# Optimization experiments

Measured on AMD Instinct MI355X. Metric: run time of the kernel, lower is better.

Reference implementation:

```python
import jax, jax.numpy as jnp
import numpy as np

B, T, D_IN, H = 32, 2048, 512, 512


def setup_inputs() -> dict:
    key = jax.random.key(0)
    ks = jax.random.split(key, 5)
    limit_z = float(np.sqrt(6.0 / (D_IN + H)))  # xavier_uniform
    return {
        "x": jax.random.normal(ks[0], (B, T, D_IN), dtype=jnp.float32),
        "motion_mag": jax.random.uniform(ks[1], (B, T), dtype=jnp.float32),
        "Wz": jax.random.uniform(ks[2], (H, D_IN), minval=-limit_z, maxval=limit_z, dtype=jnp.float32),
        "bz": jnp.full((H,), -2.0, dtype=jnp.float32),
        "Wh": jax.random.uniform(ks[3], (H, D_IN), minval=-limit_z, maxval=limit_z, dtype=jnp.float32),
        "bh": jnp.zeros((H,), dtype=jnp.float32),
        "motion_weight": jnp.asarray(1.0, dtype=jnp.float32),
        "motion_bias": jnp.asarray(0.0, dtype=jnp.float32),
        "alpha": jnp.asarray(0.5, dtype=jnp.float32),
    }


def reference(x, motion_mag, Wz, bz, Wh, bh, motion_weight, motion_bias, alpha):
    # motion-conditioned gate temperature: (B, T, 1)
    a = jax.nn.softplus(alpha)
    tau = 1.0 + a * jax.nn.sigmoid(motion_weight * motion_mag + motion_bias)
    tau = tau[..., None]
    # parallel gate / candidate projections
    z = jax.nn.sigmoid((jnp.einsum('btd,hd->bth', x, Wz) + bz) / tau)  # (B,T,H)
    h_tilde = jnp.einsum('btd,hd->bth', x, Wh) + bh                     # (B,T,H)
    # sequential elementwise recurrence: h = (1-z)*h + z*h_tilde
    h0 = jnp.zeros((x.shape[0], Wz.shape[0]), dtype=x.dtype)

    def step(h, zt_ht):
        z_t, ht_t = zt_ht
        h = (1.0 - z_t) * h + z_t * ht_t
        return h, h

    _, outs = jax.lax.scan(step, h0, (jnp.swapaxes(z, 0, 1), jnp.swapaxes(h_tilde, 0, 1)))
    return jnp.swapaxes(outs, 0, 1)  # (B, T, H)
```

## Files before the change

kernel.cpp:

```cpp
#include <hip/hip_runtime.h>
#include <math.h>

#define BATCH 32
#define TLEN 2048
#define DIN 512
#define HDIM 512
#define BTROWS (BATCH * TLEN)

typedef __attribute__((ext_vector_type(8))) short short8;
typedef __attribute__((ext_vector_type(4))) float f32x4;

__device__ __forceinline__ float sigmoidf_(float v) {
    return 1.0f / (1.0f + __expf(-v));
}

__device__ __forceinline__ unsigned short bf16_rne(float f) {
    unsigned int u = __float_as_uint(f);
    u += 0x7FFFu + ((u >> 16) & 1u);
    return (unsigned short)(u >> 16);
}

__device__ __forceinline__ void conv_body(const float* src, int t, size_t tile,
                                          short* Hs, short* Ls,
                                          short* __restrict__ dhi, short* __restrict__ dlo) {
    const int row = t >> 1, half = t & 1;
    float v[16];
#pragma unroll
    for (int i = 0; i < 4; ++i)
        *(float4*)&v[i * 4] = *(const float4*)(src + i * 4);
    const int s = row >> 4, r = row & 15;
#pragma unroll
    for (int jj = 0; jj < 2; ++jj) {
        short8 hv, lv;
#pragma unroll
        for (int e = 0; e < 8; ++e) {
            const float f = v[jj * 8 + e];
            const unsigned short h = bf16_rne(f);
            const float hf = __uint_as_float(((unsigned int)h) << 16);
            hv[e] = (short)h;
            lv[e] = (short)bf16_rne(f - hf);
        }
        const int idx = s * 512 + (half * 2 + jj) * 128 + r * 8;
        *(short8*)&Hs[idx] = hv;
        *(short8*)&Ls[idx] = lv;
    }
    __syncthreads();
    const size_t ob = tile * 4096 + (size_t)t * 16;
    *(short8*)(dhi + ob)     = *(short8*)&Hs[t * 16];
    *(short8*)(dhi + ob + 8) = *(short8*)&Hs[t * 16 + 8];
    *(short8*)(dlo + ob)     = *(short8*)&Ls[t * 16];
    *(short8*)(dlo + ob + 8) = *(short8*)&Ls[t * 16 + 8];
}

__global__ __launch_bounds__(256) void convert_x_kernel(const float* __restrict__ x,
                                                        short* __restrict__ xhi,
                                                        short* __restrict__ xlo) {
    __shared__ short Hs[4096], Ls[4096];
    const int tile = blockIdx.x;
    const int rt = tile >> 4, kt = tile & 15;
    const int t = threadIdx.x;
    const int row = t >> 1, half = t & 1;
    const float* src = x + (size_t)(rt * 128 + row) * DIN + kt * 32 + half * 16;
    conv_body(src, t, (size_t)tile, Hs, Ls, xhi, xlo);
}

__global__ __launch_bounds__(256) void convert_w_kernel(const float* __restrict__ Wz,
                                                        const float* __restrict__ Wh,
                                                        short* __restrict__ whi,
                                                        short* __restrict__ wlo) {
    __shared__ short Hs[4096], Ls[4096];
    const int tile = blockIdx.x;
    const int ct = tile >> 4, kt = tile & 15;
    const int t = threadIdx.x;
    const int row = t >> 1, half = t & 1;
    const int wrow = ct * 128 + row;
    const float* base = (wrow < HDIM) ? (Wz + (size_t)wrow * DIN)
                                      : (Wh + (size_t)(wrow - HDIM) * DIN);
    const float* src = base + kt * 32 + half * 16;
    conv_body(src, t, (size_t)tile, Hs, Ls, whi, wlo);
}

#define GLOAD16(g, l) __builtin_amdgcn_global_load_lds(                         \
    (const __attribute__((address_space(1))) unsigned int*)(g),                 \
    (__attribute__((address_space(3))) unsigned int*)(l), 16, 0, 0)

__global__ __launch_bounds__(256) void gemm_mfma_kernel(
    const short* __restrict__ xhi, const short* __restrict__ xlo,
    const short* __restrict__ whi, const short* __restrict__ wlo,
    const float* __restrict__ bz, const float* __restrict__ bh,
    const float* __restrict__ mag,
    const float* __restrict__ mw_p, const float* __restrict__ mb_p,
    const float* __restrict__ al_p,
    float* __restrict__ zbuf, float* __restrict__ out)
{
    __shared__ short Ah[4096], Al[4096], Bh[4096], Bl[4096];

    const int orig = blockIdx.x;
    const int xcd = orig & 7, idx = orig >> 3;
    const int wg = xcd * 512 + idx;
    const int bj = wg & 7;
    const int bi = wg >> 3;

    const int tid = threadIdx.x;
    const int w = tid >> 6, l = tid & 63;
    const int wr = w >> 1, wc = w & 1;

    f32x4 acc[4][4];
#pragma unroll
    for (int i = 0; i < 4; ++i)
#pragma unroll
        for (int j = 0; j < 4; ++j) acc[i][j] = (f32x4)0.f;

    const size_t ab = (size_t)bi * (16 * 4096);
    const size_t bb = (size_t)bj * (16 * 4096);
    const int c0 = tid, c1 = tid + 256;
    const int lb0 = (w * 64) * 8;
    const int lb1 = (256 + w * 64) * 8;

    for (int kt = 0; kt < 16; ++kt) {
        const size_t ta = ab + (size_t)kt * 4096;
        const size_t tb = bb + (size_t)kt * 4096;
        GLOAD16(xhi + ta + c0 * 8, &Ah[lb0]);
        GLOAD16(xhi + ta + c1 * 8, &Ah[lb1]);
        GLOAD16(xlo + ta + c0 * 8, &Al[lb0]);
        GLOAD16(xlo + ta + c1 * 8, &Al[lb1]);
        GLOAD16(whi + tb + c0 * 8, &Bh[lb0]);
        GLOAD16(whi + tb + c1 * 8, &Bh[lb1]);
        GLOAD16(wlo + tb + c0 * 8, &Bl[lb0]);
        GLOAD16(wlo + tb + c1 * 8, &Bl[lb1]);
        __syncthreads();

        short8 av[4], aw[4], bv[4], bw[4];
#pragma unroll
        for (int i = 0; i < 4; ++i) {
            av[i] = *(const short8*)&Ah[(wr * 4 + i) * 512 + l * 8];
            aw[i] = *(const short8*)&Al[(wr * 4 + i) * 512 + l * 8];
            bv[i] = *(const short8*)&Bh[(wc * 4 + i) * 512 + l * 8];
            bw[i] = *(const short8*)&Bl[(wc * 4 + i) * 512 + l * 8];
        }
#pragma unroll
        for (int i = 0; i < 4; ++i)
#pragma unroll
            for (int j = 0; j < 4; ++j) {
                acc[i][j] = __builtin_amdgcn_mfma_f32_16x16x32_bf16(av[i], bv[j], acc[i][j], 0, 0, 0);
                acc[i][j] = __builtin_amdgcn_mfma_f32_16x16x32_bf16(aw[i], bv[j], acc[i][j], 0, 0, 0);
                acc[i][j] = __builtin_amdgcn_mfma_f32_16x16x32_bf16(av[i], bw[j], acc[i][j], 0, 0, 0);
            }
        __syncthreads();
    }

    const float mwv = *mw_p, mbv = *mb_p, alv = *al_p;
    const float asp = fmaxf(alv, 0.f) + log1pf(__expf(-fabsf(alv)));
    const int colbase = bj * 128 + wc * 64 + (l & 15);
    const int rowbase = bi * 128 + wr * 64 + ((l >> 4) << 2);

    if (bj < 4) {
        float itau[4][4];
#pragma unroll
        for (int i = 0; i < 4; ++i)
#pragma unroll
            for (int q = 0; q < 4; ++q) {
                const int row = rowbase + i * 16 + q;
                const float tau = 1.0f + asp * sigmoidf_(mwv * mag[row] + mbv);
                itau[i][q] = 1.0f / tau;
            }
#pragma unroll
        for (int j = 0; j < 4; ++j) {
            const int col = colbase + j * 16;
            const float bzv = bz[col];
#pragma unroll
            for (int i = 0; i < 4; ++i)
#pragma unroll
                for (int q = 0; q < 4; ++q) {
                    const int row = rowbase + i * 16 + q;
                    zbuf[(size_t)row * HDIM + col] = sigmoidf_((acc[i][j][q] + bzv) * itau[i][q]);
                }
        }
    } else {
#pragma unroll
        for (int j = 0; j < 4; ++j) {
            const int col = colbase + j * 16 - HDIM;
            const float bhv = bh[col];
#pragma unroll
            for (int i = 0; i < 4; ++i)
#pragma unroll
                for (int q = 0; q < 4; ++q) {
                    const int row = rowbase + i * 16 + q;
                    out[(size_t)row * HDIM + col] = acc[i][j][q] + bhv;
                }
        }
    }
}

#define BM 128
#define BN 128
#define BK 16
#define TM 8
#define TN 8

__global__ __launch_bounds__(256) void gemm_dual_kernel(
    const float* __restrict__ x, const float* __restrict__ Wz, const float* __restrict__ Wh,
    const float* __restrict__ bz, const float* __restrict__ bh, const float* __restrict__ mag,
    const float* __restrict__ mw_p, const float* __restrict__ mb_p, const float* __restrict__ al_p,
    float* __restrict__ zbuf, float* __restrict__ htbuf)
{
    __shared__ float As[BK][BM + 4];
    __shared__ float Zs[BK][BN + 4];
    __shared__ float Hs[BK][BN + 4];

    const int bj = blockIdx.x, bi = blockIdx.y;
    const int tid = threadIdx.x;
    const int tx = tid & 15, ty = tid >> 4;
    const int row0 = bi * BM, col0 = bj * BN;

    float accZ[TM][TN], accH[TM][TN];
#pragma unroll
    for (int i = 0; i < TM; ++i)
#pragma unroll
        for (int j = 0; j < TN; ++j) { accZ[i][j] = 0.f; accH[i][j] = 0.f; }

    const int srow = tid >> 1;
    const int skc = (tid & 1) * 8;
    const float* xg = x + (size_t)(row0 + srow) * DIN + skc;
    const float* wzg = Wz + (size_t)(col0 + srow) * DIN + skc;
    const float* whg = Wh + (size_t)(col0 + srow) * DIN + skc;

    for (int k0 = 0; k0 < DIN; k0 += BK) {
        const float4 a0 = *(const float4*)(xg + k0);
        const float4 a1 = *(const float4*)(xg + k0 + 4);
        const float4 z0 = *(const float4*)(wzg + k0);
        const float4 z1 = *(const float4*)(wzg + k0 + 4);
        const float4 h0 = *(const float4*)(whg + k0);
        const float4 h1 = *(const float4*)(whg + k0 + 4);
        __syncthreads();
        As[skc + 0][srow] = a0.x; As[skc + 1][srow] = a0.y; As[skc + 2][srow] = a0.z; As[skc + 3][srow] = a0.w;
        As[skc + 4][srow] = a1.x; As[skc + 5][srow] = a1.y; As[skc + 6][srow] = a1.z; As[skc + 7][srow] = a1.w;
        Zs[skc + 0][srow] = z0.x; Zs[skc + 1][srow] = z0.y; Zs[skc + 2][srow] = z0.z; Zs[skc + 3][srow] = z0.w;
        Zs[skc + 4][srow] = z1.x; Zs[skc + 5][srow] = z1.y; Zs[skc + 6][srow] = z1.z; Zs[skc + 7][srow] = z1.w;
        Hs[skc + 0][srow] = h0.x; Hs[skc + 1][srow] = h0.y; Hs[skc + 2][srow] = h0.z; Hs[skc + 3][srow] = h0.w;
        Hs[skc + 4][srow] = h1.x; Hs[skc + 5][srow] = h1.y; Hs[skc + 6][srow] = h1.z; Hs[skc + 7][srow] = h1.w;
        __syncthreads();
#pragma unroll
        for (int kk = 0; kk < BK; ++kk) {
            const float4 av0 = *(const float4*)&As[kk][ty * TM];
            const float4 av1 = *(const float4*)&As[kk][ty * TM + 4];
            const float4 zv0 = *(const float4*)&Zs[kk][tx * TN];
            const float4 zv1 = *(const float4*)&Zs[kk][tx * TN + 4];
            const float4 hv0 = *(const float4*)&Hs[kk][tx * TN];
            const float4 hv1 = *(const float4*)&Hs[kk][tx * TN + 4];
            const float a[TM] = {av0.x, av0.y, av0.z, av0.w, av1.x, av1.y, av1.z, av1.w};
            const float zw[TN] = {zv0.x, zv0.y, zv0.z, zv0.w, zv1.x, zv1.y, zv1.z, zv1.w};
            const float hw[TN] = {hv0.x, hv0.y, hv0.z, hv0.w, hv1.x, hv1.y, hv1.z, hv1.w};
#pragma unroll
            for (int i = 0; i < TM; ++i)
#pragma unroll
                for (int j = 0; j < TN; ++j) {
                    accZ[i][j] = fmaf(a[i], zw[j], accZ[i][j]);
                    accH[i][j] = fmaf(a[i], hw[j], accH[i][j]);
                }
        }
    }

    const float mwv = *mw_p, mbv = *mb_p, alv = *al_p;
    const float asp = fmaxf(alv, 0.f) + log1pf(__expf(-fabsf(alv)));
    float bzv[TN], bhv[TN];
#pragma unroll
    for (int j = 0; j < TN; ++j) {
        bzv[j] = bz[col0 + tx * TN + j];
        bhv[j] = bh[col0 + tx * TN + j];
    }
#pragma unroll
    for (int i = 0; i < TM; ++i) {
        const int r = row0 + ty * TM + i;
        const float tau = 1.0f + asp * sigmoidf_(mwv * mag[r] + mbv);
        const float itau = 1.0f / tau;
        float zo[TN], ho[TN];
#pragma unroll
        for (int j = 0; j < TN; ++j) {
            zo[j] = sigmoidf_((accZ[i][j] + bzv[j]) * itau);
            ho[j] = accH[i][j] + bhv[j];
        }
        float* zp = zbuf + (size_t)r * HDIM + col0 + tx * TN;
        float* hp = htbuf + (size_t)r * HDIM + col0 + tx * TN;
        *(float4*)(zp) = make_float4(zo[0], zo[1], zo[2], zo[3]);
        *(float4*)(zp + 4) = make_float4(zo[4], zo[5], zo[6], zo[7]);
        *(float4*)(hp) = make_float4(ho[0], ho[1], ho[2], ho[3]);
        *(float4*)(hp + 4) = make_float4(ho[4], ho[5], ho[6], ho[7]);
    }
}

__global__ __launch_bounds__(64) void scan_kernel(
    const float* __restrict__ zb, float* __restrict__ hio)
{
    const int u = blockIdx.x * 64 + threadIdx.x;
    const int b = u >> 9;
    const int h = u & 511;
    const size_t base = (size_t)b * (size_t)(TLEN * HDIM) + h;
    const float* zp = zb + base;
    float* hp = hio + base;

    float hprev = 0.f;
    float zA[16], hA[16], zB[16], hB[16];
#pragma unroll
    for (int k = 0; k < 16; ++k) {
        zA[k] = zp[(size_t)k * HDIM];
        hA[k] = hp[(size_t)k * HDIM];
    }
    for (int t0 = 0; t0 < TLEN; t0 += 32) {
#pragma unroll
        for (int k = 0; k < 16; ++k) {
            zB[k] = zp[(size_t)(t0 + 16 + k) * HDIM];
            hB[k] = hp[(size_t)(t0 + 16 + k) * HDIM];
        }
#pragma unroll
        for (int k = 0; k < 16; ++k) {
            hprev = fmaf(zA[k], hA[k] - hprev, hprev);
            hp[(size_t)(t0 + k) * HDIM] = hprev;
        }
        if (t0 + 32 < TLEN) {
#pragma unroll
            for (int k = 0; k < 16; ++k) {
                zA[k] = zp[(size_t)(t0 + 32 + k) * HDIM];
                hA[k] = hp[(size_t)(t0 + 32 + k) * HDIM];
            }
        }
#pragma unroll
        for (int k = 0; k < 16; ++k) {
            hprev = fmaf(zB[k], hB[k] - hprev, hprev);
            hp[(size_t)(t0 + 16 + k) * HDIM] = hprev;
        }
    }
}

extern "C" void kernel_launch(void* const* d_in, const int* in_sizes, int n_in,
                              void* d_out, int out_size, void* d_ws, size_t ws_size,
                              hipStream_t stream) {
    const float* x   = (const float*)d_in[0];
    const float* mag = (const float*)d_in[1];
    const float* Wz  = (const float*)d_in[2];
    const float* bz  = (const float*)d_in[3];
    const float* Wh  = (const float*)d_in[4];
    const float* bh  = (const float*)d_in[5];
    const float* mw  = (const float*)d_in[6];
    const float* mb  = (const float*)d_in[7];
    const float* al  = (const float*)d_in[8];

    float* out = (float*)d_out;
    char* ws = (char*)d_ws;

    const size_t Z_BYTES  = (size_t)BTROWS * HDIM * 4;
    const size_t XP_BYTES = (size_t)BTROWS * DIN * 2;
    const size_t WP_BYTES = (size_t)(2 * HDIM) * DIN * 2;
    const size_t NEED = Z_BYTES + 2 * XP_BYTES + 2 * WP_BYTES;

    float* zbuf = (float*)ws;

    if (ws_size >= NEED) {
        short* xhi = (short*)(ws + Z_BYTES);
        short* xlo = (short*)(ws + Z_BYTES + XP_BYTES);
        short* whi = (short*)(ws + Z_BYTES + 2 * XP_BYTES);
        short* wlo = (short*)(ws + Z_BYTES + 2 * XP_BYTES + WP_BYTES);

        convert_x_kernel<<<8192, 256, 0, stream>>>(x, xhi, xlo);
        convert_w_kernel<<<128, 256, 0, stream>>>(Wz, Wh, whi, wlo);
        gemm_mfma_kernel<<<4096, 256, 0, stream>>>(xhi, xlo, whi, wlo,
                                                   bz, bh, mag, mw, mb, al, zbuf, out);
    } else {
        dim3 grid(HDIM / BN, BTROWS / BM);
        gemm_dual_kernel<<<grid, 256, 0, stream>>>(x, Wz, Wh, bz, bh, mag, mw, mb, al, zbuf, out);
    }

    scan_kernel<<<BATCH * HDIM / 64, 64, 0, stream>>>(zbuf, out);
}
```

Measured before the change: 615.1 us.

## Double-buffer GEMM LDS tiles, deepen scan prefetch, drop LDS staging in convert

The GEMM main loop now uses two LDS buffers per operand, so the global-to-LDS load of the next K tile overlaps the MFMA work on the current one. It also raises wave priority around the MFMA block. The scan kernel prefetches 32 timesteps per buffer instead of 16, giving more memory-level parallelism at the cost of more registers. The convert kernels write the swizzled bf16 hi/lo tiles straight to global memory instead of staging them through shared memory, which removes a barrier but makes the stores less coalesced.

```diff
diff --git a/kernel.cpp b/kernel.cpp
--- a/kernel.cpp
+++ b/kernel.cpp
@@ -20,15 +20,17 @@
     return (unsigned short)(u >> 16);
 }
 
-__device__ __forceinline__ void conv_body(const float* src, int t, size_t tile,
-                                          short* Hs, short* Ls,
-                                          short* __restrict__ dhi, short* __restrict__ dlo) {
+__device__ __forceinline__ void conv_store(const float* __restrict__ src,
+                                           int t, size_t tile,
+                                           short* __restrict__ dhi,
+                                           short* __restrict__ dlo) {
     const int row = t >> 1, half = t & 1;
+    const int s = row >> 4, r = row & 15;
     float v[16];
 #pragma unroll
     for (int i = 0; i < 4; ++i)
         *(float4*)&v[i * 4] = *(const float4*)(src + i * 4);
-    const int s = row >> 4, r = row & 15;
+    const size_t ob = tile * 4096;
 #pragma unroll
     for (int jj = 0; jj < 2; ++jj) {
         short8 hv, lv;
@@ -41,34 +43,26 @@
             lv[e] = (short)bf16_rne(f - hf);
         }
         const int idx = s * 512 + (half * 2 + jj) * 128 + r * 8;
-        *(short8*)&Hs[idx] = hv;
-        *(short8*)&Ls[idx] = lv;
-    }
-    __syncthreads();
-    const size_t ob = tile * 4096 + (size_t)t * 16;
-    *(short8*)(dhi + ob)     = *(short8*)&Hs[t * 16];
-    *(short8*)(dhi + ob + 8) = *(short8*)&Hs[t * 16 + 8];
-    *(short8*)(dlo + ob)     = *(short8*)&Ls[t * 16];
-    *(short8*)(dlo + ob + 8) = *(short8*)&Ls[t * 16 + 8];
+        *(short8*)(dhi + ob + idx) = hv;
+        *(short8*)(dlo + ob + idx) = lv;
+    }
 }
 
 __global__ __launch_bounds__(256) void convert_x_kernel(const float* __restrict__ x,
                                                         short* __restrict__ xhi,
                                                         short* __restrict__ xlo) {
-    __shared__ short Hs[4096], Ls[4096];
     const int tile = blockIdx.x;
     const int rt = tile >> 4, kt = tile & 15;
     const int t = threadIdx.x;
     const int row = t >> 1, half = t & 1;
     const float* src = x + (size_t)(rt * 128 + row) * DIN + kt * 32 + half * 16;
-    conv_body(src, t, (size_t)tile, Hs, Ls, xhi, xlo);
+    conv_store(src, t, (size_t)tile, xhi, xlo);
 }
 
 __global__ __launch_bounds__(256) void convert_w_kernel(const float* __restrict__ Wz,
                                                         const float* __restrict__ Wh,
                                                         short* __restrict__ whi,
                                                         short* __restrict__ wlo) {
-    __shared__ short Hs[4096], Ls[4096];
     const int tile = blockIdx.x;
     const int ct = tile >> 4, kt = tile & 15;
     const int t = threadIdx.x;
@@ -77,7 +71,7 @@
     const float* base = (wrow < HDIM) ? (Wz + (size_t)wrow * DIN)
                                       : (Wh + (size_t)(wrow - HDIM) * DIN);
     const float* src = base + kt * 32 + half * 16;
-    conv_body(src, t, (size_t)tile, Hs, Ls, whi, wlo);
+    conv_store(src, t, (size_t)tile, whi, wlo);
 }
 
 #define GLOAD16(g, l) __builtin_amdgcn_global_load_lds(                         \
@@ -93,7 +87,7 @@
     const float* __restrict__ al_p,
     float* __restrict__ zbuf, float* __restrict__ out)
 {
-    __shared__ short Ah[4096], Al[4096], Bh[4096], Bl[4096];
+    __shared__ short Ah[2][4096], Al[2][4096], Bh[2][4096], Bl[2][4096];
 
     const int orig = blockIdx.x;
     const int xcd = orig & 7, idx = orig >> 3;
@@ -117,27 +111,35 @@
     const int lb0 = (w * 64) * 8;
     const int lb1 = (256 + w * 64) * 8;
 
+#define STAGE(buf, kt) do {                                                     \
+        const size_t ta_ = ab + (size_t)(kt) * 4096;                            \
+        const size_t tb_ = bb + (size_t)(kt) * 4096;                            \
+        GLOAD16(xhi + ta_ + c0 * 8, &Ah[buf][lb0]);                             \
+        GLOAD16(xhi + ta_ + c1 * 8, &Ah[buf][lb1]);                             \
+        GLOAD16(xlo + ta_ + c0 * 8, &Al[buf][lb0]);                             \
+        GLOAD16(xlo + ta_ + c1 * 8, &Al[buf][lb1]);                             \
+        GLOAD16(whi + tb_ + c0 * 8, &Bh[buf][lb0]);                             \
+        GLOAD16(whi + tb_ + c1 * 8, &Bh[buf][lb1]);                             \
+        GLOAD16(wlo + tb_ + c0 * 8, &Bl[buf][lb0]);                             \
+        GLOAD16(wlo + tb_ + c1 * 8, &Bl[buf][lb1]);                             \
+    } while (0)
+
+    STAGE(0, 0);
+    __syncthreads();
+
     for (int kt = 0; kt < 16; ++kt) {
-        const size_t ta = ab + (size_t)kt * 4096;
-        const size_t tb = bb + (size_t)kt * 4096;
-        GLOAD16(xhi + ta + c0 * 8, &Ah[lb0]);
-        GLOAD16(xhi + ta + c1 * 8, &Ah[lb1]);
-        GLOAD16(xlo + ta + c0 * 8, &Al[lb0]);
-        GLOAD16(xlo + ta + c1 * 8, &Al[lb1]);
-        GLOAD16(whi + tb + c0 * 8, &Bh[lb0]);
-        GLOAD16(whi + tb + c1 * 8, &Bh[lb1]);
-        GLOAD16(wlo + tb + c0 * 8, &Bl[lb0]);
-        GLOAD16(wlo + tb + c1 * 8, &Bl[lb1]);
-        __syncthreads();
+        const int cur = kt & 1;
+        if (kt < 15) STAGE(cur ^ 1, kt + 1);
 
         short8 av[4], aw[4], bv[4], bw[4];
 #pragma unroll
         for (int i = 0; i < 4; ++i) {
-            av[i] = *(const short8*)&Ah[(wr * 4 + i) * 512 + l * 8];
-            aw[i] = *(const short8*)&Al[(wr * 4 + i) * 512 + l * 8];
-            bv[i] = *(const short8*)&Bh[(wc * 4 + i) * 512 + l * 8];
-            bw[i] = *(const short8*)&Bl[(wc * 4 + i) * 512 + l * 8];
-        }
+            av[i] = *(const short8*)&Ah[cur][(wr * 4 + i) * 512 + l * 8];
+            aw[i] = *(const short8*)&Al[cur][(wr * 4 + i) * 512 + l * 8];
+            bv[i] = *(const short8*)&Bh[cur][(wc * 4 + i) * 512 + l * 8];
+            bw[i] = *(const short8*)&Bl[cur][(wc * 4 + i) * 512 + l * 8];
+        }
+        __builtin_amdgcn_s_setprio(1);
 #pragma unroll
         for (int i = 0; i < 4; ++i)
 #pragma unroll
@@ -146,8 +148,10 @@
                 acc[i][j] = __builtin_amdgcn_mfma_f32_16x16x32_bf16(aw[i], bv[j], acc[i][j], 0, 0, 0);
                 acc[i][j] = __builtin_amdgcn_mfma_f32_16x16x32_bf16(av[i], bw[j], acc[i][j], 0, 0, 0);
             }
+        __builtin_amdgcn_s_setprio(0);
         __syncthreads();
     }
+#undef STAGE
 
     const float mwv = *mw_p, mbv = *mb_p, alv = *al_p;
     const float asp = fmaxf(alv, 0.f) + log1pf(__expf(-fabsf(alv)));
@@ -293,41 +297,39 @@
     const float* __restrict__ zb, float* __restrict__ hio)
 {
     const int u = blockIdx.x * 64 + threadIdx.x;
-    const int b = u >> 9;
-    const int h = u & 511;
-    const size_t base = (size_t)b * (size_t)(TLEN * HDIM) + h;
+    const size_t base = ((size_t)(u >> 9) * (size_t)(TLEN * HDIM)) + (u & 511);
     const float* zp = zb + base;
     float* hp = hio + base;
 
     float hprev = 0.f;
-    float zA[16], hA[16], zB[16], hB[16];
-#pragma unroll
-    for (int k = 0; k < 16; ++k) {
+    float zA[32], hA[32], zB[32], hB[32];
+#pragma unroll
+    for (int k = 0; k < 32; ++k) {
         zA[k] = zp[(size_t)k * HDIM];
         hA[k] = hp[(size_t)k * HDIM];
     }
-    for (int t0 = 0; t0 < TLEN; t0 += 32) {
-#pragma unroll
-        for (int k = 0; k < 16; ++k) {
-            zB[k] = zp[(size_t)(t0 + 16 + k) * HDIM];
-            hB[k] = hp[(size_t)(t0 + 16 + k) * HDIM];
-        }
-#pragma unroll
-        for (int k = 0; k < 16; ++k) {
+    for (int t0 = 0; t0 < TLEN; t0 += 64) {
+#pragma unroll
+        for (int k = 0; k < 32; ++k) {
+            zB[k] = zp[(size_t)(t0 + 32 + k) * HDIM];
+            hB[k] = hp[(size_t)(t0 + 32 + k) * HDIM];
+        }
+#pragma unroll
+        for (int k = 0; k < 32; ++k) {
             hprev = fmaf(zA[k], hA[k] - hprev, hprev);
             hp[(size_t)(t0 + k) * HDIM] = hprev;
         }
-        if (t0 + 32 < TLEN) {
-#pragma unroll
-            for (int k = 0; k < 16; ++k) {
-                zA[k] = zp[(size_t)(t0 + 32 + k) * HDIM];
-                hA[k] = hp[(size_t)(t0 + 32 + k) * HDIM];
+        if (t0 + 64 < TLEN) {
+#pragma unroll
+            for (int k = 0; k < 32; ++k) {
+                zA[k] = zp[(size_t)(t0 + 64 + k) * HDIM];
+                hA[k] = hp[(size_t)(t0 + 64 + k) * HDIM];
             }
         }
 #pragma unroll
-        for (int k = 0; k < 16; ++k) {
+        for (int k = 0; k < 32; ++k) {
             hprev = fmaf(zB[k], hB[k] - hprev, hprev);
-            hp[(size_t)(t0 + 16 + k) * HDIM] = hprev;
+            hp[(size_t)(t0 + 32 + k) * HDIM] = hprev;
         }
     }
 }
```

New measurement: 598.1 us. 2.8% less time.
